# Performance work log

Hardware: AMD Instinct MI355X
Metric: run time of the kernel (lower is better)

## Reference

```python
import jax, jax.numpy as jnp
import numpy as np

TOP_K = 512  # int(node_num * K) = int(2048 * 0.25)
NEG = -1.0e12
SLOPE = 0.01  # nn.LeakyReLU default negative_slope


def setup_inputs() -> dict:
    key = jax.random.key(0)
    k1, k2, k3, k4 = jax.random.split(key, 4)
    B, N, in_c, out_c, gs = 8, 2048, 128, 128, 128
    x = jax.random.normal(k1, (B, N, in_c), dtype=jnp.float32)
    W = jax.random.normal(k2, (in_c, out_c), dtype=jnp.float32) * (1.0 / np.sqrt(in_c))
    a = jax.random.normal(k3, (2 * out_c, 1), dtype=jnp.float32) * (1.0 / np.sqrt(2 * out_c))
    GL = jax.random.normal(k4, (N, gs), dtype=jnp.float32) * (1.0 / np.sqrt(gs))
    return {"x": x, "W": W, "a": a, "GL": GL}


def reference(x, W, a, GL):
    B, N, _ = x.shape
    out_c = W.shape[1]
    # learned adjacency: softmax(relu(GL GL^T)) + I  -> [N, N]
    adj = jax.nn.softmax(jax.nn.relu(GL @ GL.T), axis=-1) + jnp.eye(N, dtype=GL.dtype)
    h = x @ W  # [B, N, out_c]
    # e[b,i,j] = LeakyReLU( [h_i ; h_j] . a ) = LeakyReLU( h_i.a1 + h_j.a2 )
    # (avoids materializing the [B, N*N, 2*out_c] concat of the original)
    a1, a2 = a[:out_c, 0], a[out_c:, 0]
    e = jax.nn.leaky_relu((h @ a1)[:, :, None] + (h @ a2)[:, None, :], SLOPE)  # [B,N,N]
    att = jnp.where(adj[None] > 0, e, NEG)
    # top-k along dim=1 (rows, per column j): transpose so that axis is last
    att_t = jnp.swapaxes(att, 1, 2)  # [B, Nj, Ni]
    _, idx = jax.lax.top_k(att_t, TOP_K)  # idx: [B, Nj, TOP_K]
    b_ix = jnp.arange(B)[:, None, None]
    j_ix = jnp.arange(N)[None, :, None]
    mask_t = jnp.zeros_like(att_t).at[b_ix, j_ix, idx].set(1.0)
    mask = jnp.swapaxes(mask_t, 1, 2)  # [B, Ni, Nj]
    att = jax.nn.softmax(att * mask, axis=2)
    h_prime = jax.nn.relu(att @ h)  # [B, N, out_c]
    return jnp.swapaxes(h_prime, -2, -1)  # [B, out_c, N]
```

## Files before the change

kernel.cpp:

```cpp
#include <hip/hip_runtime.h>
#include <math.h>


#define B_ 8
#define N_ 2048
#define C_ 128
#define TOPK_ 512
#define NCH_ 32
#define CL_ 64
#define NP1_ 2052
#define RANKB_ 256

#define H_OFF    ((size_t)0)
#define P_OFF    (H_OFF + (size_t)B_*N_*C_)
#define Q_OFF    (P_OFF + (size_t)B_*N_)
#define LOK_OFF  (Q_OFF + (size_t)B_*N_)
#define US_OFF   (LOK_OFF + (size_t)B_*N_)
#define VS_OFF   (US_OFF + (size_t)B_*N_)
#define SRT_OFF  (VS_OFF + (size_t)B_*N_)
#define SUS_OFF  (SRT_OFF + (size_t)B_*N_)
#define PVS_OFF  (SUS_OFF + (size_t)B_*NP1_)
#define SUL_OFF  (PVS_OFF + (size_t)B_*NP1_)
#define PVL_OFF  (SUL_OFF + (size_t)B_*N_*128)
#define TOTU_OFF (PVL_OFF + (size_t)B_*N_*128)
#define TOTV_OFF (TOTU_OFF + (size_t)B_*NCH_*128)
#define MPART_OFF (TOTV_OFF + (size_t)B_*NCH_*128)

__global__ __launch_bounds__(256) void k_pq(const float* __restrict__ x,
                                            const float* __restrict__ W,
                                            const float* __restrict__ a,
                                            float* __restrict__ p,
                                            float* __restrict__ q) {
  __shared__ float al[256];
  __shared__ float wa1[128], wa2[128];
  const int t = threadIdx.x;
  const int r0 = blockIdx.x * 64;
  al[t] = a[t];
  __syncthreads();
  if (t < 128) {
    const float* Wr = W + (size_t)t * 128;
    float s1 = 0.f, s2 = 0.f;
#pragma unroll
    for (int j = 0; j < 128; j += 4) {
      float4 wv = *(const float4*)(Wr + j);
      s1 = fmaf(wv.x, al[j + 0], s1);
      s1 = fmaf(wv.y, al[j + 1], s1);
      s1 = fmaf(wv.z, al[j + 2], s1);
      s1 = fmaf(wv.w, al[j + 3], s1);
      s2 = fmaf(wv.x, al[128 + j + 0], s2);
      s2 = fmaf(wv.y, al[128 + j + 1], s2);
      s2 = fmaf(wv.z, al[128 + j + 2], s2);
      s2 = fmaf(wv.w, al[128 + j + 3], s2);
    }
    wa1[t] = s1; wa2[t] = s2;
  }
  __syncthreads();
  const int row = t >> 2, part = t & 3;
  const float* xr = x + (size_t)(r0 + row) * 128 + part * 32;
  const float* w1 = wa1 + part * 32;
  const float* w2 = wa2 + part * 32;
  float sp = 0.f, sq = 0.f;
#pragma unroll
  for (int i = 0; i < 8; ++i) {
    float4 xv = *(const float4*)(xr + 4 * i);
    float4 w1v = *(const float4*)(w1 + 4 * i);
    float4 w2v = *(const float4*)(w2 + 4 * i);
    sp = fmaf(xv.x, w1v.x, sp); sp = fmaf(xv.y, w1v.y, sp);
    sp = fmaf(xv.z, w1v.z, sp); sp = fmaf(xv.w, w1v.w, sp);
    sq = fmaf(xv.x, w2v.x, sq); sq = fmaf(xv.y, w2v.y, sq);
    sq = fmaf(xv.z, w2v.z, sq); sq = fmaf(xv.w, w2v.w, sq);
  }
  sp += __shfl_xor(sp, 1, 64); sp += __shfl_xor(sp, 2, 64);
  sq += __shfl_xor(sq, 1, 64); sq += __shfl_xor(sq, 2, 64);
  if (part == 0) { p[r0 + row] = sp; q[r0 + row] = sq; }
}

__global__ __launch_bounds__(512, 4) void k_fuse(
    const float* __restrict__ x, const float* __restrict__ W,
    float* __restrict__ h, float* __restrict__ mpart,
    const float* __restrict__ q, const float* __restrict__ p,
    float* __restrict__ u_s, float* __restrict__ v_s,
    int* __restrict__ srt, int* __restrict__ lok) {
  union __align__(16) SMem {
    struct { float Wl[64 * 128]; float xl[64 * 68]; } g;
    struct { float ql[N_]; float pl[N_]; } r;
  };
  __shared__ SMem sm;
  const int blk = blockIdx.x, t = threadIdx.x;

  if (blk < RANKB_) {
    const int b = blk >> 5, tile = blk & 31;
    const int i0 = tile * 64;
    ((float4*)sm.r.ql)[t] = ((const float4*)(q + (size_t)b * N_))[t];
    ((float4*)sm.r.pl)[t] = ((const float4*)(p + (size_t)b * N_))[t];
    __syncthreads();
    const int row = t >> 3, s = t & 7;
    const int i = i0 + row;
    const float qi = sm.r.ql[i], pi = sm.r.pl[i];
    const float negpi = -pi;
    int qr = 0, lo = 0, pr = 0;
    for (int g = s; g < 512; g += 8) {
      float4 qj = ((const float4*)sm.r.ql)[g];
      float4 pj = ((const float4*)sm.r.pl)[g];
      const int j0 = 4 * g;
      qr += (qj.x < qi || (qj.x == qi && (j0 + 0) < i)) ? 1 : 0;
      qr += (qj.y < qi || (qj.y == qi && (j0 + 1) < i)) ? 1 : 0;
      qr += (qj.z < qi || (qj.z == qi && (j0 + 2) < i)) ? 1 : 0;
      qr += (qj.w < qi || (qj.w == qi && (j0 + 3) < i)) ? 1 : 0;
      lo += (qj.x < negpi) ? 1 : 0;
      lo += (qj.y < negpi) ? 1 : 0;
      lo += (qj.z < negpi) ? 1 : 0;
      lo += (qj.w < negpi) ? 1 : 0;
      pr += (pj.x > pi || (pj.x == pi && (j0 + 0) < i)) ? 1 : 0;
      pr += (pj.y > pi || (pj.y == pi && (j0 + 1) < i)) ? 1 : 0;
      pr += (pj.z > pi || (pj.z == pi && (j0 + 2) < i)) ? 1 : 0;
      pr += (pj.w > pi || (pj.w == pi && (j0 + 3) < i)) ? 1 : 0;
    }
    qr += __shfl_xor(qr, 1, 64); qr += __shfl_xor(qr, 2, 64); qr += __shfl_xor(qr, 4, 64);
    lo += __shfl_xor(lo, 1, 64); lo += __shfl_xor(lo, 2, 64); lo += __shfl_xor(lo, 4, 64);
    pr += __shfl_xor(pr, 1, 64); pr += __shfl_xor(pr, 2, 64); pr += __shfl_xor(pr, 4, 64);
    if (s == 0) {
      u_s[(size_t)b * N_ + qr] = __expf(qi);
      v_s[(size_t)b * N_ + qr] = __expf(0.01f * qi);
      srt[(size_t)b * N_ + qr] = i;
      lok[(size_t)b * N_ + i] = lo | ((pr < TOPK_) ? 0x10000 : 0);
    }
    return;
  }

  float* Wl = sm.g.Wl;
  float* xl = sm.g.xl;
  const int g = blk - RANKB_;
  const int r0 = g * 64;
  const int cg = t & 15, rp = (t >> 4) & 15;
  const bool act = t < 256;
  float acc[4][8];
#pragma unroll
  for (int r = 0; r < 4; ++r)
#pragma unroll
    for (int j = 0; j < 8; ++j) acc[r][j] = 0.f;

  for (int kc = 0; kc < 2; ++kc) {
    __syncthreads();
    const float4* W4 = (const float4*)(W + (size_t)kc * 64 * 128);
    float4* Wl4 = (float4*)Wl;
#pragma unroll
    for (int i = 0; i < 4; ++i) Wl4[t + 512 * i] = W4[t + 512 * i];
#pragma unroll
    for (int i = 0; i < 2; ++i) {
      int idx = t + 512 * i;
      int row = idx >> 4, c4i = idx & 15;
      float4 v = *(const float4*)(x + (size_t)(r0 + row) * 128 + kc * 64 + c4i * 4);
      ((float4*)xl)[row * 17 + c4i] = v;
    }
    __syncthreads();
    if (act) {
      for (int k = 0; k < 64; ++k) {
        const float4* Wr = (const float4*)(Wl + k * 128);
        float4 w0 = Wr[cg];
        float4 w1 = Wr[cg + 16];
#pragma unroll
        for (int r = 0; r < 4; ++r) {
          float xv = xl[(4 * rp + r) * 68 + k];
          acc[r][0] = fmaf(xv, w0.x, acc[r][0]);
          acc[r][1] = fmaf(xv, w0.y, acc[r][1]);
          acc[r][2] = fmaf(xv, w0.z, acc[r][2]);
          acc[r][3] = fmaf(xv, w0.w, acc[r][3]);
          acc[r][4] = fmaf(xv, w1.x, acc[r][4]);
          acc[r][5] = fmaf(xv, w1.y, acc[r][5]);
          acc[r][6] = fmaf(xv, w1.z, acc[r][6]);
          acc[r][7] = fmaf(xv, w1.w, acc[r][7]);
        }
      }
    }
  }
  const int c0 = 4 * cg, c1 = 4 * cg + 64;
  size_t hb = (size_t)r0 * 128;
  __syncthreads();
  float* scratch = xl;
  if (act) {
#pragma unroll
    for (int r = 0; r < 4; ++r) {
      int row = 4 * rp + r;
      *(float4*)(h + hb + (size_t)row * 128 + c0) =
          make_float4(acc[r][0], acc[r][1], acc[r][2], acc[r][3]);
      *(float4*)(h + hb + (size_t)row * 128 + c1) =
          make_float4(acc[r][4], acc[r][5], acc[r][6], acc[r][7]);
    }
#pragma unroll
    for (int j = 0; j < 4; ++j) {
      scratch[rp * 128 + c0 + j] = acc[0][j] + acc[1][j] + acc[2][j] + acc[3][j];
      scratch[rp * 128 + c1 + j] = acc[0][4 + j] + acc[1][4 + j] + acc[2][4 + j] + acc[3][4 + j];
    }
  }
  __syncthreads();
  if (t < 128) {
    float s = 0.f;
#pragma unroll
    for (int rr = 0; rr < 16; ++rr) s += scratch[rr * 128 + t];
    mpart[(size_t)g * 128 + t] = s;
  }
}

__global__ __launch_bounds__(256) void k_scan(const float* __restrict__ h,
                                              const float* __restrict__ u_s,
                                              const float* __restrict__ v_s,
                                              const int* __restrict__ srt,
                                              float* __restrict__ SUl,
                                              float* __restrict__ PVl,
                                              float* __restrict__ totU,
                                              float* __restrict__ totV,
                                              float* __restrict__ SUS,
                                              float* __restrict__ PVS) {
  __shared__ float hl[CL_][128];
  __shared__ float ul[CL_], vl[CL_];
  __shared__ int sl[CL_];
  __shared__ float2 sa[256], sb[256];
  const int t = threadIdx.x;
  if (blockIdx.x >= 256) {
    const int b = blockIdx.x - 256;
    float4 ua = ((const float4*)(u_s + (size_t)b * N_))[2 * t];
    float4 ub = ((const float4*)(u_s + (size_t)b * N_))[2 * t + 1];
    float4 wa = ((const float4*)(v_s + (size_t)b * N_))[2 * t];
    float4 wb = ((const float4*)(v_s + (size_t)b * N_))[2 * t + 1];
    float su = ua.x + ua.y + ua.z + ua.w + ub.x + ub.y + ub.z + ub.w;
    float sw = wa.x + wa.y + wa.z + wa.w + wb.x + wb.y + wb.z + wb.w;
    sa[t] = make_float2(su, sw);
    __syncthreads();
    float2* cur = sa; float2* nxt = sb;
    for (int off = 1; off < 256; off <<= 1) {
      float2 vv = cur[t];
      if (t >= off) { float2 o = cur[t - off]; vv.x += o.x; vv.y += o.y; }
      nxt[t] = vv;
      __syncthreads();
      float2* tmp = cur; cur = nxt; nxt = tmp;
    }
    float2 incl = cur[t];
    float2 tot = cur[255];
    float exclU = incl.x - su, exclW = incl.y - sw;
    float s0 = tot.x - exclU;
    float s1 = s0 - ua.x, s2 = s1 - ua.y, s3 = s2 - ua.z;
    float s4 = s3 - ua.w, s5 = s4 - ub.x, s6 = s5 - ub.y, s7 = s6 - ub.z;
    float p0 = exclW;
    float p1 = p0 + wa.x, p2 = p1 + wa.y, p3 = p2 + wa.z;
    float p4 = p3 + wa.w, p5 = p4 + wb.x, p6 = p5 + wb.y, p7 = p6 + wb.z;
    float* Sb = SUS + (size_t)b * NP1_ + 8 * t;
    float* Pb = PVS + (size_t)b * NP1_ + 8 * t;
    *(float4*)(Sb) = make_float4(s0, s1, s2, s3);
    *(float4*)(Sb + 4) = make_float4(s4, s5, s6, s7);
    *(float4*)(Pb) = make_float4(p0, p1, p2, p3);
    *(float4*)(Pb + 4) = make_float4(p4, p5, p6, p7);
    if (t == 255) {
      SUS[(size_t)b * NP1_ + N_] = 0.f;
      PVS[(size_t)b * NP1_ + N_] = tot.y;
    }
    return;
  }
  const int b = blockIdx.x >> 5, ch = blockIdx.x & 31;
  const int base = b * N_ + ch * CL_;
  if (t < CL_) { ul[t] = u_s[base + t]; vl[t] = v_s[base + t]; sl[t] = srt[base + t]; }
  __syncthreads();
  {
    const int c4 = t & 31, rr = t >> 5;
#pragma unroll
    for (int i = 0; i < 8; ++i) {
      int tt = rr + 8 * i;
      float4 v = *(const float4*)(h + ((size_t)b * N_ + sl[tt]) * 128 + 4 * c4);
      *(float4*)(&hl[tt][4 * c4]) = v;
    }
  }
  __syncthreads();
  if (t < 128) {
    const int c = t;
    float run = 0.f;
    for (int tt = CL_ - 1; tt >= 0; --tt) {
      run = fmaf(ul[tt], hl[tt][c], run);
      SUl[((size_t)(base + tt)) * 128 + c] = run;
    }
    totU[(size_t)(b * NCH_ + ch) * 128 + c] = run;
  } else {
    const int c = t - 128;
    float run2 = 0.f;
    for (int tt = 0; tt < CL_; ++tt) {
      PVl[((size_t)(base + tt)) * 128 + c] = run2;
      run2 = fmaf(vl[tt], hl[tt][c], run2);
    }
    totV[(size_t)(b * NCH_ + ch) * 128 + c] = run2;
  }
}

__global__ __launch_bounds__(256) void k_out(const float* __restrict__ p,
                                             const int* __restrict__ lok,
                                             const float* __restrict__ SUS,
                                             const float* __restrict__ PVS,
                                             const float* __restrict__ SUl,
                                             const float* __restrict__ PVl,
                                             const float* __restrict__ totU,
                                             const float* __restrict__ totV,
                                             const float* __restrict__ mpart,
                                             float* __restrict__ out) {
  __shared__ float res[64 * 129];
  __shared__ float CSUs[(NCH_ + 1) * 128];
  __shared__ float CPVs[(NCH_ + 1) * 128];
  __shared__ float mr[128];
  __shared__ float A_s[64], B_s[64], invD[64];
  __shared__ int lo_s[64], keep_s[64];
  const int b = blockIdx.x >> 5, tile = blockIdx.x & 31;
  const int t = threadIdx.x;
  const int i0 = tile * 64;
  if (t < 128) {
    float ms = 0.f;
#pragma unroll
    for (int j = 0; j < 32; ++j) ms += mpart[(size_t)(b * 32 + j) * 128 + t];
    mr[t] = fmaxf(ms * (1.0f / (float)N_), 0.f);
    float s = 0.f;
    CSUs[NCH_ * 128 + t] = 0.f;
    for (int cc = NCH_ - 1; cc >= 0; --cc) {
      s += totU[(size_t)(b * NCH_ + cc) * 128 + t];
      CSUs[cc * 128 + t] = s;
    }
  } else {
    const int c2 = t - 128;
    float s2 = 0.f;
    for (int cc = 0; cc < NCH_; ++cc) {
      CPVs[cc * 128 + c2] = s2;
      s2 += totV[(size_t)(b * NCH_ + cc) * 128 + c2];
    }
    CPVs[NCH_ * 128 + c2] = s2;
  }
  __syncthreads();
  if (t < 64) {
    float pv = p[b * N_ + i0 + t];
    int lk = lok[(size_t)b * N_ + i0 + t];
    keep_s[t] = (lk >> 16) & 1;
    int lo = lk & 0xFFFF;
    lo_s[t] = lo;
    float A = __expf(pv), Bv = __expf(0.01f * pv);
    A_s[t] = A; B_s[t] = Bv;
    float sus = SUS[(size_t)b * NP1_ + lo];
    float pvs = PVS[(size_t)b * NP1_ + lo];
    invD[t] = 1.0f / fmaf(A, sus, Bv * pvs);
  }
  __syncthreads();
  const int half = t >> 7, c = t & 127;
#pragma unroll 4
  for (int ii2 = 0; ii2 < 64; ii2 += 2) {
    int ii = ii2 + half;
    float outv;
    if (keep_s[ii]) {
      int lo = lo_s[ii];
      float A = A_s[ii], Bv = B_s[ii];
      float suc, pvc;
      if (lo < N_) {
        int chn = lo >> 6;
        size_t ro = ((size_t)(b * N_ + lo)) * 128;
        suc = SUl[ro + c] + CSUs[(chn + 1) * 128 + c];
        pvc = PVl[ro + c] + CPVs[chn * 128 + c];
      } else {
        suc = 0.f;
        pvc = CPVs[NCH_ * 128 + c];
      }
      outv = fmaxf(fmaf(A, suc, Bv * pvc) * invD[ii], 0.f);
    } else {
      outv = mr[c];
    }
    res[ii * 129 + c] = outv;
  }
  __syncthreads();
#pragma unroll
  for (int pass = 0; pass < 8; ++pass) {
    int cc = (t >> 4) + pass * 16;
    int ii4 = (t & 15) * 4;
    float4 v;
    v.x = res[(ii4 + 0) * 129 + cc];
    v.y = res[(ii4 + 1) * 129 + cc];
    v.z = res[(ii4 + 2) * 129 + cc];
    v.w = res[(ii4 + 3) * 129 + cc];
    *(float4*)(out + ((size_t)(b * C_ + cc)) * N_ + i0 + ii4) = v;
  }
}

extern "C" void kernel_launch(void* const* d_in, const int* in_sizes, int n_in,
                              void* d_out, int out_size, void* d_ws, size_t ws_size,
                              hipStream_t stream) {
  (void)in_sizes; (void)n_in; (void)out_size; (void)ws_size;
  const float* x = (const float*)d_in[0];
  const float* W = (const float*)d_in[1];
  const float* a = (const float*)d_in[2];
  float* out = (float*)d_out;
  float* ws = (float*)d_ws;

  float* h    = ws + H_OFF;
  float* p    = ws + P_OFF;
  float* q    = ws + Q_OFF;
  int*   lok  = (int*)(ws + LOK_OFF);
  float* u_s  = ws + US_OFF;
  float* v_s  = ws + VS_OFF;
  int*   srt  = (int*)(ws + SRT_OFF);
  float* SUS  = ws + SUS_OFF;
  float* PVS  = ws + PVS_OFF;
  float* SUl  = ws + SUL_OFF;
  float* PVl  = ws + PVL_OFF;
  float* totU = ws + TOTU_OFF;
  float* totV = ws + TOTV_OFF;
  float* mpart = ws + MPART_OFF;

  k_pq<<<dim3((B_ * N_) / 64), dim3(256), 0, stream>>>(x, W, a, p, q);
  k_fuse<<<dim3(RANKB_ + (B_ * N_) / 64), dim3(512), 0, stream>>>(
      x, W, h, mpart, q, p, u_s, v_s, srt, lok);
  k_scan<<<dim3(256 + B_), dim3(256), 0, stream>>>(h, u_s, v_s, srt, SUl, PVl, totU, totV, SUS, PVS);
  k_out<<<dim3(B_ * 32), dim3(256), 0, stream>>>(p, lok, SUS, PVS, SUl, PVl, totU, totV, mpart, out);
}
```

Measured before the change: 104.3 us.

## Fuse p/q projection, GEMM and ranking into one kernel with redundant p/q compute

Merges the separate p/q projection kernel and the split GEMM/ranking kernel into a single 256-block kernel. Each block first computes its 64-row tile of h=xW and the column partial sums, then recomputes p and q for its whole batch (2048 rows) into shared memory and ranks its 64 rows. This removes one launch and the global round trip for q, at the cost of each block rereading all of x for its batch. The GEMM and the ranking now run one after the other inside each block instead of on separate blocks.

```diff
diff --git a/kernel.cpp b/kernel.cpp
--- a/kernel.cpp
+++ b/kernel.cpp
@@ -9,12 +9,11 @@
 #define NCH_ 32
 #define CL_ 64
 #define NP1_ 2052
-#define RANKB_ 256
+#define GRID1_ 256
 
 #define H_OFF    ((size_t)0)
 #define P_OFF    (H_OFF + (size_t)B_*N_*C_)
-#define Q_OFF    (P_OFF + (size_t)B_*N_)
-#define LOK_OFF  (Q_OFF + (size_t)B_*N_)
+#define LOK_OFF  (P_OFF + (size_t)B_*N_)
 #define US_OFF   (LOK_OFF + (size_t)B_*N_)
 #define VS_OFF   (US_OFF + (size_t)B_*N_)
 #define SRT_OFF  (VS_OFF + (size_t)B_*N_)
@@ -26,16 +25,94 @@
 #define TOTV_OFF (TOTU_OFF + (size_t)B_*NCH_*128)
 #define MPART_OFF (TOTV_OFF + (size_t)B_*NCH_*128)
 
-__global__ __launch_bounds__(256) void k_pq(const float* __restrict__ x,
-                                            const float* __restrict__ W,
-                                            const float* __restrict__ a,
-                                            float* __restrict__ p,
-                                            float* __restrict__ q) {
-  __shared__ float al[256];
-  __shared__ float wa1[128], wa2[128];
-  const int t = threadIdx.x;
-  const int r0 = blockIdx.x * 64;
-  al[t] = a[t];
+__global__ __launch_bounds__(512, 4) void k_gvr(
+    const float* __restrict__ x, const float* __restrict__ W,
+    const float* __restrict__ a,
+    float* __restrict__ h, float* __restrict__ mpart, float* __restrict__ p,
+    float* __restrict__ u_s, float* __restrict__ v_s,
+    int* __restrict__ srt, int* __restrict__ lok) {
+  union SM {
+    struct { float Wl[64 * 128]; float xl[64 * 68]; } g;
+    struct { float ql[N_]; float pl[N_];
+             float wa1[128]; float wa2[128]; float al[256]; } r;
+  };
+  __shared__ SM sm;
+  const int blk = blockIdx.x, t = threadIdx.x;
+  const int b = blk >> 5, tile = blk & 31;
+  const int r0 = blk * 64;
+
+  const int cg2 = t & 15, rp = (t >> 4) & 15;
+  const bool act = t < 256;
+  float acc[4][8];
+#pragma unroll
+  for (int r = 0; r < 4; ++r)
+#pragma unroll
+    for (int j = 0; j < 8; ++j) acc[r][j] = 0.f;
+  for (int kc = 0; kc < 2; ++kc) {
+    __syncthreads();
+    const float4* W4 = (const float4*)(W + (size_t)kc * 64 * 128);
+    float4* Wl4 = (float4*)sm.g.Wl;
+#pragma unroll
+    for (int i = 0; i < 4; ++i) Wl4[t + 512 * i] = W4[t + 512 * i];
+#pragma unroll
+    for (int i = 0; i < 2; ++i) {
+      int idx = t + 512 * i;
+      int row = idx >> 4, c4i = idx & 15;
+      float4 v = *(const float4*)(x + (size_t)(r0 + row) * 128 + kc * 64 + c4i * 4);
+      ((float4*)sm.g.xl)[row * 17 + c4i] = v;
+    }
+    __syncthreads();
+    if (act) {
+      for (int k = 0; k < 64; ++k) {
+        const float4* Wr = (const float4*)(sm.g.Wl + k * 128);
+        float4 w0 = Wr[cg2];
+        float4 w1 = Wr[cg2 + 16];
+#pragma unroll
+        for (int r = 0; r < 4; ++r) {
+          float xv = sm.g.xl[(4 * rp + r) * 68 + k];
+          acc[r][0] = fmaf(xv, w0.x, acc[r][0]);
+          acc[r][1] = fmaf(xv, w0.y, acc[r][1]);
+          acc[r][2] = fmaf(xv, w0.z, acc[r][2]);
+          acc[r][3] = fmaf(xv, w0.w, acc[r][3]);
+          acc[r][4] = fmaf(xv, w1.x, acc[r][4]);
+          acc[r][5] = fmaf(xv, w1.y, acc[r][5]);
+          acc[r][6] = fmaf(xv, w1.z, acc[r][6]);
+          acc[r][7] = fmaf(xv, w1.w, acc[r][7]);
+        }
+      }
+    }
+  }
+  {
+    const int c0 = 4 * cg2, c1 = 4 * cg2 + 64;
+    size_t hb = (size_t)r0 * 128;
+    __syncthreads();
+    float* scratch = sm.g.xl;
+    if (act) {
+#pragma unroll
+      for (int r = 0; r < 4; ++r) {
+        int row = 4 * rp + r;
+        *(float4*)(h + hb + (size_t)row * 128 + c0) =
+            make_float4(acc[r][0], acc[r][1], acc[r][2], acc[r][3]);
+        *(float4*)(h + hb + (size_t)row * 128 + c1) =
+            make_float4(acc[r][4], acc[r][5], acc[r][6], acc[r][7]);
+      }
+#pragma unroll
+      for (int j = 0; j < 4; ++j) {
+        scratch[rp * 128 + c0 + j] = acc[0][j] + acc[1][j] + acc[2][j] + acc[3][j];
+        scratch[rp * 128 + c1 + j] = acc[0][4 + j] + acc[1][4 + j] + acc[2][4 + j] + acc[3][4 + j];
+      }
+    }
+    __syncthreads();
+    if (t < 128) {
+      float s = 0.f;
+#pragma unroll
+      for (int rr = 0; rr < 16; ++rr) s += scratch[rr * 128 + t];
+      mpart[(size_t)blk * 128 + t] = s;
+    }
+  }
+  __syncthreads();
+
+  if (t < 256) sm.r.al[t] = a[t];
   __syncthreads();
   if (t < 128) {
     const float* Wr = W + (size_t)t * 128;
@@ -43,66 +120,59 @@
 #pragma unroll
     for (int j = 0; j < 128; j += 4) {
       float4 wv = *(const float4*)(Wr + j);
-      s1 = fmaf(wv.x, al[j + 0], s1);
-      s1 = fmaf(wv.y, al[j + 1], s1);
-      s1 = fmaf(wv.z, al[j + 2], s1);
-      s1 = fmaf(wv.w, al[j + 3], s1);
-      s2 = fmaf(wv.x, al[128 + j + 0], s2);
-      s2 = fmaf(wv.y, al[128 + j + 1], s2);
-      s2 = fmaf(wv.z, al[128 + j + 2], s2);
-      s2 = fmaf(wv.w, al[128 + j + 3], s2);
-    }
-    wa1[t] = s1; wa2[t] = s2;
-  }
-  __syncthreads();
-  const int row = t >> 2, part = t & 3;
-  const float* xr = x + (size_t)(r0 + row) * 128 + part * 32;
-  const float* w1 = wa1 + part * 32;
-  const float* w2 = wa2 + part * 32;
-  float sp = 0.f, sq = 0.f;
-#pragma unroll
-  for (int i = 0; i < 8; ++i) {
-    float4 xv = *(const float4*)(xr + 4 * i);
-    float4 w1v = *(const float4*)(w1 + 4 * i);
-    float4 w2v = *(const float4*)(w2 + 4 * i);
-    sp = fmaf(xv.x, w1v.x, sp); sp = fmaf(xv.y, w1v.y, sp);
-    sp = fmaf(xv.z, w1v.z, sp); sp = fmaf(xv.w, w1v.w, sp);
-    sq = fmaf(xv.x, w2v.x, sq); sq = fmaf(xv.y, w2v.y, sq);
-    sq = fmaf(xv.z, w2v.z, sq); sq = fmaf(xv.w, w2v.w, sq);
-  }
-  sp += __shfl_xor(sp, 1, 64); sp += __shfl_xor(sp, 2, 64);
-  sq += __shfl_xor(sq, 1, 64); sq += __shfl_xor(sq, 2, 64);
-  if (part == 0) { p[r0 + row] = sp; q[r0 + row] = sq; }
-}
-
-__global__ __launch_bounds__(512, 4) void k_fuse(
-    const float* __restrict__ x, const float* __restrict__ W,
-    float* __restrict__ h, float* __restrict__ mpart,
-    const float* __restrict__ q, const float* __restrict__ p,
-    float* __restrict__ u_s, float* __restrict__ v_s,
-    int* __restrict__ srt, int* __restrict__ lok) {
-  union __align__(16) SMem {
-    struct { float Wl[64 * 128]; float xl[64 * 68]; } g;
-    struct { float ql[N_]; float pl[N_]; } r;
-  };
-  __shared__ SMem sm;
-  const int blk = blockIdx.x, t = threadIdx.x;
-
-  if (blk < RANKB_) {
-    const int b = blk >> 5, tile = blk & 31;
+      s1 = fmaf(wv.x, sm.r.al[j + 0], s1);
+      s1 = fmaf(wv.y, sm.r.al[j + 1], s1);
+      s1 = fmaf(wv.z, sm.r.al[j + 2], s1);
+      s1 = fmaf(wv.w, sm.r.al[j + 3], s1);
+      s2 = fmaf(wv.x, sm.r.al[128 + j + 0], s2);
+      s2 = fmaf(wv.y, sm.r.al[128 + j + 1], s2);
+      s2 = fmaf(wv.z, sm.r.al[128 + j + 2], s2);
+      s2 = fmaf(wv.w, sm.r.al[128 + j + 3], s2);
+    }
+    sm.r.wa1[t] = s1; sm.r.wa2[t] = s2;
+  }
+  __syncthreads();
+  {
+    const int row8 = t >> 3, part = t & 7;
+    const float* xb = x + (size_t)b * N_ * 128;
+    const float* w1 = sm.r.wa1 + part * 16;
+    const float* w2 = sm.r.wa2 + part * 16;
+    for (int pass = 0; pass < 32; ++pass) {
+      const int r = pass * 64 + row8;
+      const float* xr = xb + (size_t)r * 128 + part * 16;
+      float sp = 0.f, sq = 0.f;
+#pragma unroll
+      for (int i2 = 0; i2 < 4; ++i2) {
+        float4 xv = *(const float4*)(xr + 4 * i2);
+        float4 w1v = *(const float4*)(w1 + 4 * i2);
+        float4 w2v = *(const float4*)(w2 + 4 * i2);
+        sp = fmaf(xv.x, w1v.x, sp); sp = fmaf(xv.y, w1v.y, sp);
+        sp = fmaf(xv.z, w1v.z, sp); sp = fmaf(xv.w, w1v.w, sp);
+        sq = fmaf(xv.x, w2v.x, sq); sq = fmaf(xv.y, w2v.y, sq);
+        sq = fmaf(xv.z, w2v.z, sq); sq = fmaf(xv.w, w2v.w, sq);
+      }
+      sp += __shfl_xor(sp, 1, 64); sp += __shfl_xor(sp, 2, 64); sp += __shfl_xor(sp, 4, 64);
+      sq += __shfl_xor(sq, 1, 64); sq += __shfl_xor(sq, 2, 64); sq += __shfl_xor(sq, 4, 64);
+      if (part == 0) {
+        sm.r.pl[r] = sp;
+        sm.r.ql[r] = sq;
+        if (tile == 0) p[(size_t)b * N_ + r] = sp;
+      }
+    }
+  }
+  __syncthreads();
+
+  {
     const int i0 = tile * 64;
-    ((float4*)sm.r.ql)[t] = ((const float4*)(q + (size_t)b * N_))[t];
-    ((float4*)sm.r.pl)[t] = ((const float4*)(p + (size_t)b * N_))[t];
-    __syncthreads();
-    const int row = t >> 3, s = t & 7;
+    const int row = t >> 3, s8 = t & 7;
     const int i = i0 + row;
     const float qi = sm.r.ql[i], pi = sm.r.pl[i];
     const float negpi = -pi;
     int qr = 0, lo = 0, pr = 0;
-    for (int g = s; g < 512; g += 8) {
-      float4 qj = ((const float4*)sm.r.ql)[g];
-      float4 pj = ((const float4*)sm.r.pl)[g];
-      const int j0 = 4 * g;
+    for (int g2 = s8; g2 < 512; g2 += 8) {
+      float4 qj = ((const float4*)sm.r.ql)[g2];
+      float4 pj = ((const float4*)sm.r.pl)[g2];
+      const int j0 = 4 * g2;
       qr += (qj.x < qi || (qj.x == qi && (j0 + 0) < i)) ? 1 : 0;
       qr += (qj.y < qi || (qj.y == qi && (j0 + 1) < i)) ? 1 : 0;
       qr += (qj.z < qi || (qj.z == qi && (j0 + 2) < i)) ? 1 : 0;
@@ -119,86 +189,12 @@
     qr += __shfl_xor(qr, 1, 64); qr += __shfl_xor(qr, 2, 64); qr += __shfl_xor(qr, 4, 64);
     lo += __shfl_xor(lo, 1, 64); lo += __shfl_xor(lo, 2, 64); lo += __shfl_xor(lo, 4, 64);
     pr += __shfl_xor(pr, 1, 64); pr += __shfl_xor(pr, 2, 64); pr += __shfl_xor(pr, 4, 64);
-    if (s == 0) {
+    if (s8 == 0) {
       u_s[(size_t)b * N_ + qr] = __expf(qi);
       v_s[(size_t)b * N_ + qr] = __expf(0.01f * qi);
       srt[(size_t)b * N_ + qr] = i;
       lok[(size_t)b * N_ + i] = lo | ((pr < TOPK_) ? 0x10000 : 0);
     }
-    return;
-  }
-
-  float* Wl = sm.g.Wl;
-  float* xl = sm.g.xl;
-  const int g = blk - RANKB_;
-  const int r0 = g * 64;
-  const int cg = t & 15, rp = (t >> 4) & 15;
-  const bool act = t < 256;
-  float acc[4][8];
-#pragma unroll
-  for (int r = 0; r < 4; ++r)
-#pragma unroll
-    for (int j = 0; j < 8; ++j) acc[r][j] = 0.f;
-
-  for (int kc = 0; kc < 2; ++kc) {
-    __syncthreads();
-    const float4* W4 = (const float4*)(W + (size_t)kc * 64 * 128);
-    float4* Wl4 = (float4*)Wl;
-#pragma unroll
-    for (int i = 0; i < 4; ++i) Wl4[t + 512 * i] = W4[t + 512 * i];
-#pragma unroll
-    for (int i = 0; i < 2; ++i) {
-      int idx = t + 512 * i;
-      int row = idx >> 4, c4i = idx & 15;
-      float4 v = *(const float4*)(x + (size_t)(r0 + row) * 128 + kc * 64 + c4i * 4);
-      ((float4*)xl)[row * 17 + c4i] = v;
-    }
-    __syncthreads();
-    if (act) {
-      for (int k = 0; k < 64; ++k) {
-        const float4* Wr = (const float4*)(Wl + k * 128);
-        float4 w0 = Wr[cg];
-        float4 w1 = Wr[cg + 16];
-#pragma unroll
-        for (int r = 0; r < 4; ++r) {
-          float xv = xl[(4 * rp + r) * 68 + k];
-          acc[r][0] = fmaf(xv, w0.x, acc[r][0]);
-          acc[r][1] = fmaf(xv, w0.y, acc[r][1]);
-          acc[r][2] = fmaf(xv, w0.z, acc[r][2]);
-          acc[r][3] = fmaf(xv, w0.w, acc[r][3]);
-          acc[r][4] = fmaf(xv, w1.x, acc[r][4]);
-          acc[r][5] = fmaf(xv, w1.y, acc[r][5]);
-          acc[r][6] = fmaf(xv, w1.z, acc[r][6]);
-          acc[r][7] = fmaf(xv, w1.w, acc[r][7]);
-        }
-      }
-    }
-  }
-  const int c0 = 4 * cg, c1 = 4 * cg + 64;
-  size_t hb = (size_t)r0 * 128;
-  __syncthreads();
-  float* scratch = xl;
-  if (act) {
-#pragma unroll
-    for (int r = 0; r < 4; ++r) {
-      int row = 4 * rp + r;
-      *(float4*)(h + hb + (size_t)row * 128 + c0) =
-          make_float4(acc[r][0], acc[r][1], acc[r][2], acc[r][3]);
-      *(float4*)(h + hb + (size_t)row * 128 + c1) =
-          make_float4(acc[r][4], acc[r][5], acc[r][6], acc[r][7]);
-    }
-#pragma unroll
-    for (int j = 0; j < 4; ++j) {
-      scratch[rp * 128 + c0 + j] = acc[0][j] + acc[1][j] + acc[2][j] + acc[3][j];
-      scratch[rp * 128 + c1 + j] = acc[0][4 + j] + acc[1][4 + j] + acc[2][4 + j] + acc[3][4 + j];
-    }
-  }
-  __syncthreads();
-  if (t < 128) {
-    float s = 0.f;
-#pragma unroll
-    for (int rr = 0; rr < 16; ++rr) s += scratch[rr * 128 + t];
-    mpart[(size_t)g * 128 + t] = s;
   }
 }
 
@@ -392,7 +388,6 @@
 
   float* h    = ws + H_OFF;
   float* p    = ws + P_OFF;
-  float* q    = ws + Q_OFF;
   int*   lok  = (int*)(ws + LOK_OFF);
   float* u_s  = ws + US_OFF;
   float* v_s  = ws + VS_OFF;
@@ -405,9 +400,7 @@
   float* totV = ws + TOTV_OFF;
   float* mpart = ws + MPART_OFF;
 
-  k_pq<<<dim3((B_ * N_) / 64), dim3(256), 0, stream>>>(x, W, a, p, q);
-  k_fuse<<<dim3(RANKB_ + (B_ * N_) / 64), dim3(512), 0, stream>>>(
-      x, W, h, mpart, q, p, u_s, v_s, srt, lok);
+  k_gvr<<<dim3(GRID1_), dim3(512), 0, stream>>>(x, W, a, h, mpart, p, u_s, v_s, srt, lok);
   k_scan<<<dim3(256 + B_), dim3(256), 0, stream>>>(h, u_s, v_s, srt, SUl, PVl, totU, totV, SUS, PVS);
   k_out<<<dim3(B_ * 32), dim3(256), 0, stream>>>(p, lok, SUS, PVS, SUl, PVl, totU, totV, mpart, out);
 }
```

Measured after the change: 125.0 us. +19.8%, slower.
